# Kernel tuning notes

Measured on AMD Instinct MI355X. Metric: run time of the kernel, lower is better.

The kernel has to match this reference:

```python
import jax, jax.numpy as jnp
import numpy as np

C_IN = 96          # spectral bands
D2 = 2 * C_IN      # d = 192 (inner dim)
D4 = 4 * D2        # 768 (4-directional scan channels)
N = 16             # SSM state size
DR = 6             # delta_rank = ceil(96/16)
B, H, W = 2, 96, 96  # H,W not in {8,16,32,64} -> s=1 path


def setup_inputs() -> dict:
    key = jax.random.key(0)
    ks = jax.random.split(key, 8)
    g = lambda k, shape, s: jax.random.normal(k, shape, jnp.float32) * s
    return {
        "x": jax.random.normal(ks[0], (B, C_IN, H, W), jnp.float32),
        "W_in": g(ks[1], (C_IN, 2 * D2), 0.05),          # in_proj (in,out)
        "b_in": jnp.zeros((2 * D2,), jnp.float32),
        "w_dw": g(ks[2], (D2, 1, 3, 3), 0.1),            # depthwise conv OIHW
        "b_dw": jnp.zeros((D2,), jnp.float32),
        "A_log": jnp.log(jnp.tile(jnp.arange(1.0, N + 1.0, dtype=jnp.float32), (D4, 1))),
        "Dp": jnp.ones((D4,), jnp.float32),
        "W_x": g(ks[3], (D4, DR + 2 * N), 0.05),         # x_proj, no bias
        "W_delta": g(ks[4], (DR, D4), 0.1),
        "b_delta": g(ks[5], (D4,), 0.1),
        "ln_g": jnp.ones((D2,), jnp.float32),
        "ln_b": jnp.zeros((D2,), jnp.float32),
        "W_out": g(ks[6], (D2, C_IN), 0.05),             # out_proj, no bias
    }


def _selective_scan(u, delta, A, Bm, Cm, Dv):
    # u, delta: [b,L,d4]; Bm, Cm: [b,L,n]; A: [d4,n]; Dv: [d4]
    b, L, d4 = u.shape
    n = A.shape[1]

    def step(h, inps):
        u_t, dt, B_t, C_t = inps                      # [b,d4],[b,d4],[b,n],[b,n]
        dA = jnp.exp(dt[:, :, None] * A)              # [b,d4,n]
        h = dA * h + (dt * u_t)[:, :, None] * B_t[:, None, :]
        y = jnp.einsum('bdn,bn->bd', h, C_t) + Dv * u_t
        return h, y

    h0 = jnp.zeros((b, d4, n), u.dtype)
    xs = (jnp.swapaxes(u, 0, 1), jnp.swapaxes(delta, 0, 1),
          jnp.swapaxes(Bm, 0, 1), jnp.swapaxes(Cm, 0, 1))
    _, ys = jax.lax.scan(step, h0, xs)                # ys: [L,b,d4]
    return jnp.swapaxes(ys, 0, 1)                     # [b,L,d4]


def reference(x, W_in, b_in, w_dw, b_dw, A_log, Dp, W_x, W_delta, b_delta, ln_g, ln_b, W_out):
    b, c, Hh, Ww = x.shape                            # s = 1 (H not in {8,16,32,64})
    d = W_in.shape[1] // 2
    # in_proj on channel-last, chunk into x / gate z
    xz = jnp.einsum('bchw,ce->bhwe', x, W_in) + b_in  # [b,h,w,2d]
    xx, z = jnp.split(xz, 2, axis=-1)
    # depthwise conv + silu
    xc = jnp.transpose(xx, (0, 3, 1, 2))              # [b,d,h,w]
    xc = jax.lax.conv_general_dilated(
        xc, w_dw, (1, 1), 'SAME', feature_group_count=d,
        dimension_numbers=('NCHW', 'OIHW', 'NCHW')) + b_dw[None, :, None, None]
    xc = jax.nn.silu(xc)
    # 4 directional flattenings (with s=1: x1==x2 row-major, x3==x4 reversed)
    L = Hh * Ww
    flat = xc.reshape(b, d, L)
    flipped = xc[:, :, ::-1, ::-1].reshape(b, d, L)
    xl = jnp.swapaxes(jnp.concatenate([flat, flat, flipped, flipped], axis=1), 1, 2)  # [b,L,4d]
    # SSM parameterization
    A = -jnp.exp(A_log)                               # [4d,n]
    x_dbl = xl @ W_x                                  # [b,L,dr+2n]
    dr, n = W_delta.shape[0], A.shape[1]
    dt_r = x_dbl[..., :dr]
    Bm = x_dbl[..., dr:dr + n]
    Cm = x_dbl[..., dr + n:]
    delta = jax.nn.softplus(dt_r @ W_delta + b_delta)  # [b,L,4d]
    y = _selective_scan(xl, delta, A, Bm, Cm, Dp)      # [b,L,4d]
    # merge 4 directions back to spatial
    y = jnp.transpose(y.reshape(b, L, 4, d), (0, 2, 3, 1))  # [b,4,d,L]
    y1 = y[:, 0].reshape(b, d, Hh, Ww)
    y2 = y[:, 1].reshape(b, d, Hh, Ww)
    y3 = y[:, 2].reshape(b, d, Hh, Ww)[:, :, ::-1, ::-1]
    y4 = y[:, 3].reshape(b, d, Hh, Ww)[:, :, ::-1, ::-1]
    yh = jnp.transpose(y1 + y2 + y3 + y4, (0, 2, 3, 1))  # [b,h,w,d]
    # LayerNorm over d
    mu = yh.mean(-1, keepdims=True)
    var = ((yh - mu) ** 2).mean(-1, keepdims=True)
    yn = (yh - mu) * jax.lax.rsqrt(var + 1e-5) * ln_g + ln_b
    out = (yn * jax.nn.silu(z)) @ W_out               # [b,h,w,c]
    return jnp.transpose(out, (0, 3, 1, 2))           # [b,c,h,w]
```

## Files before the change

### kernel.cpp

```cpp
#include <hip/hip_runtime.h>
#include <hip/hip_bf16.h>
#include <math.h>

#define CIN 96
#define D2 192
#define D4 768
#define LL 9216
#define NN 16
#define NCH 288
#define CLEN 32

typedef float v2f __attribute__((ext_vector_type(2)));

#define SZ_Y4SLOT (2u*2u*9216u*192u)
#define SZ_BL    (2u*9216u*192u)
#define SZ_XDBL  (2u*9216u*38u)
#define SZ_S     (2u*4u*288u*192u)
#define SZ_HSLOT (2u*4u*288u*192u*8u)
#define F_Y4     0u
#define F_XX     0u
#define F_ZS     (F_Y4 + SZ_Y4SLOT)
#define F_XT     (F_ZS + SZ_BL)
#define F_XD0    (F_XT + SZ_BL)
#define F_XD1    (F_XD0 + SZ_XDBL)
#define F_XD2    (F_XD1 + SZ_XDBL)
#define F_XD3    (F_XD2 + SZ_XDBL)
#define F_SBUF   (F_XD3 + SZ_XDBL)
#define F_HBUF   (F_SBUF + SZ_S)
#define F_WCOMB  (F_HBUF + SZ_HSLOT)
#define F_A0     (F_WCOMB + 15360u)
#define F_FF     (F_A0 + 768u)

__device__ __forceinline__ float silu_f(float z) {
    return z / (1.0f + __expf(-z));
}

__global__ __launch_bounds__(256) void k0_foldw(
    const float* __restrict__ Wx, const float* __restrict__ Alog,
    float* __restrict__ wcomb, float* __restrict__ A0f, float* __restrict__ Ffl)
{
    int i = blockIdx.x * 256 + threadIdx.x;
    if (i < 768) {
        float a0 = -__expf(Alog[i * 16]);
        bool fast = true;
        for (int n = 1; n < 16; n++) {
            float an = -__expf(Alog[i * 16 + n]);
            float tgt = (n + 1) * a0;
            fast = fast && (fabsf(an - tgt) <= 1e-5f * fabsf(tgt));
        }
        A0f[i] = a0;
        Ffl[i] = fast ? 1.f : 0.f;
    }
    if (i >= 192 * 80) return;
    int d = i / 80, j = i % 80;
    float v = 0.f;
    if (j < 38) v = Wx[d * 38 + j] + Wx[(d + 192) * 38 + j];
    else if (j >= 40 && j < 78) {
        int jj = j - 40;
        v = Wx[(d + 384) * 38 + jj] + Wx[(d + 576) * 38 + jj];
    }
    wcomb[i] = v;
}

__global__ __launch_bounds__(256) void k1_inproj(
    const float* __restrict__ x, const float* __restrict__ Win,
    const float* __restrict__ bin, float* __restrict__ xx, float* __restrict__ zs)
{
    __shared__ float xs[32][68];
    __shared__ float wsh[32][100];
    int tid = threadIdx.x;
    int bid = blockIdx.x;
    int eq = bid & 3;
    int lt = (bid >> 2) % 144;
    int b = bid / 576;
    int l0 = lt * 64;
    int e0 = eq * 96;

    int lg = tid & 15;
    int cg = tid >> 4;
    v2f acc[4][3];
#pragma unroll
    for (int i = 0; i < 4; i++)
#pragma unroll
        for (int p = 0; p < 3; p++) { acc[i][p].x = 0.f; acc[i][p].y = 0.f; }

    for (int kc = 0; kc < 96; kc += 32) {
        __syncthreads();
        for (int i = tid; i < 512; i += 256) {
            int kk = i >> 4, q = i & 15;
            float4 v = *(const float4*)&x[(size_t)(b * 96 + kc + kk) * LL + l0 + q * 4];
            *(float4*)&xs[kk][q * 4] = v;
        }
        for (int i = tid; i < 768; i += 256) {
            int kk = i / 24, q = i - kk * 24;
            float4 v = *(const float4*)&Win[(kc + kk) * 384 + e0 + q * 4];
            *(float4*)&wsh[kk][q * 4] = v;
        }
        __syncthreads();
#pragma unroll 4
        for (int k = 0; k < 32; k++) {
            float4 xv = *(const float4*)&xs[k][lg * 4];
            const v2f* wp = (const v2f*)&wsh[k][cg * 6];
            v2f w0 = wp[0], w1 = wp[1], w2 = wp[2];
            float xa[4] = {xv.x, xv.y, xv.z, xv.w};
#pragma unroll
            for (int i = 0; i < 4; i++) {
                v2f xi; xi.x = xa[i]; xi.y = xa[i];
                acc[i][0] += xi * w0;
                acc[i][1] += xi * w1;
                acc[i][2] += xi * w2;
            }
        }
    }
    if (eq < 2) {
#pragma unroll
        for (int j = 0; j < 6; j++) {
            int e = e0 + cg * 6 + j;
            float bb = bin[e];
            float4 v = {acc[0][j >> 1][j & 1] + bb, acc[1][j >> 1][j & 1] + bb,
                        acc[2][j >> 1][j & 1] + bb, acc[3][j >> 1][j & 1] + bb};
            *(float4*)&xx[(size_t)(b * 192 + e) * LL + l0 + lg * 4] = v;
        }
    } else {
        int zc0 = e0 - 192 + cg * 6;
        float bb[6];
#pragma unroll
        for (int j = 0; j < 6; j++) bb[j] = bin[e0 + cg * 6 + j];
#pragma unroll
        for (int i = 0; i < 4; i++) {
            int l = l0 + lg * 4 + i;
            float* zp = &zs[((size_t)b * LL + l) * 192 + zc0];
#pragma unroll
            for (int p = 0; p < 3; p++) {
                float2 v;
                v.x = silu_f(acc[i][p].x + bb[2 * p]);
                v.y = silu_f(acc[i][p].y + bb[2 * p + 1]);
                *(float2*)&zp[2 * p] = v;
            }
        }
    }
}

__global__ __launch_bounds__(192) void k2_conv(
    const float* __restrict__ xx, const float* __restrict__ wdw,
    const float* __restrict__ bdw, float* __restrict__ xt)
{
    __shared__ float tile[32][97];
    __shared__ float wsm[32][9];
    __shared__ float bs[32];
    int tid = threadIdx.x;
    int bid = blockIdx.x;
    int h = bid % 96;
    int r = bid / 96;
    int dg = r % 6;
    int b = r / 6;

    for (int i = tid; i < 288; i += 192) wsm[i / 9][i % 9] = wdw[(dg * 32 + i / 9) * 9 + (i % 9)];
    if (tid < 32) bs[tid] = bdw[dg * 32 + tid];
    __syncthreads();

    int w = tid % 96;
    int dhalf = tid / 96;
    for (int p = 0; p < 16; p++) {
        int dsub = 2 * p + dhalf;
        const float* base = xx + (size_t)(b * 192 + dg * 32 + dsub) * LL;
        float acc = bs[dsub];
#pragma unroll
        for (int kh = 0; kh < 3; kh++) {
            int hh = h + kh - 1;
            if (hh < 0 || hh >= 96) continue;
            const float* row = base + hh * 96;
#pragma unroll
            for (int kw = 0; kw < 3; kw++) {
                int ww = w + kw - 1;
                if (ww < 0 || ww >= 96) continue;
                acc += row[ww] * wsm[dsub][kh * 3 + kw];
            }
        }
        tile[dsub][w] = silu_f(acc);
    }
    __syncthreads();
    for (int i = tid; i < 768; i += 192) {
        int q = i & 7, ls = i >> 3;
        float4 v = {tile[q * 4 + 0][ls], tile[q * 4 + 1][ls], tile[q * 4 + 2][ls], tile[q * 4 + 3][ls]};
        *(float4*)&xt[((size_t)b * LL + h * 96 + ls) * 192 + dg * 32 + q * 4] = v;
    }
}

__global__ __launch_bounds__(320) void k3_xdbl(
    const float* __restrict__ xt, const float* __restrict__ wcomb,
    float* __restrict__ xa0, float* __restrict__ xa1,
    float* __restrict__ xb0, float* __restrict__ xb1)
{
    __shared__ float xs[16][68];
    __shared__ float wsh[16][80];
    int tid = threadIdx.x;
    int bid = blockIdx.x;
    int kh = bid & 1;
    int rt = (bid >> 1) % 144;
    int b = bid / 288;
    int r0 = rt * 64;
    int k0 = kh * 96;
    float* __restrict__ xa = kh ? xa1 : xa0;
    float* __restrict__ xb = kh ? xb1 : xb0;

    int rg = tid / 20;
    int cg = tid % 20;
    v2f acc[4][2];
#pragma unroll
    for (int i = 0; i < 4; i++)
#pragma unroll
        for (int p = 0; p < 2; p++) { acc[i][p].x = 0.f; acc[i][p].y = 0.f; }

    for (int kc = 0; kc < 96; kc += 16) {
        __syncthreads();
        if (tid < 256) {
            int row = tid >> 2, dq = tid & 3;
            float4 v = *(const float4*)&xt[((size_t)b * LL + r0 + row) * 192 + k0 + kc + dq * 4];
            xs[dq * 4 + 0][row] = v.x;
            xs[dq * 4 + 1][row] = v.y;
            xs[dq * 4 + 2][row] = v.z;
            xs[dq * 4 + 3][row] = v.w;
        }
        for (int i = tid; i < 16 * 80; i += 320) {
            int d = i / 80, j = i - d * 80;
            wsh[d][j] = wcomb[(k0 + kc + d) * 80 + j];
        }
        __syncthreads();
#pragma unroll
        for (int d = 0; d < 16; d++) {
            float4 xv = *(const float4*)&xs[d][rg * 4];
            float4 wv = *(const float4*)&wsh[d][cg * 4];
            v2f w01; w01.x = wv.x; w01.y = wv.y;
            v2f w23; w23.x = wv.z; w23.y = wv.w;
            float xr[4] = {xv.x, xv.y, xv.z, xv.w};
#pragma unroll
            for (int i = 0; i < 4; i++) {
                v2f xi; xi.x = xr[i]; xi.y = xr[i];
                acc[i][0] += xi * w01;
                acc[i][1] += xi * w23;
            }
        }
    }
    int c0 = cg * 4;
#pragma unroll
    for (int i = 0; i < 4; i++) {
        int la = r0 + rg * 4 + i;
#pragma unroll
        for (int j = 0; j < 4; j++) {
            int col = c0 + j;
            float v = acc[i][j >> 1][j & 1];
            if (col < 38) {
                xa[((size_t)b * LL + la) * 38 + col] = v;
            } else if (col >= 40 && col < 78) {
                int lb = LL - 1 - la;
                xb[((size_t)b * LL + lb) * 38 + (col - 40)] = v;
            }
        }
    }
}

__global__ __launch_bounds__(192, 4) void k4_pass1(
    const float* __restrict__ xt,
    const float* __restrict__ xa0, const float* __restrict__ xa1,
    const float* __restrict__ xb0, const float* __restrict__ xb1,
    const float* __restrict__ Wd, const float* __restrict__ bdl,
    const float* __restrict__ Alog, const float* __restrict__ A0f,
    const float* __restrict__ Ffl,
    float* __restrict__ Sbuf, __hip_bfloat16* __restrict__ Hbuf)
{
    __shared__ float Bt[CLEN][16];
    __shared__ float Dt[CLEN][6];
    int tid = threadIdx.x;
    int bid = blockIdx.x;
    int k = bid % NCH;
    int r = bid / NCH;
    int dir = r & 3;
    int b = r >> 2;
    int l0 = k * CLEN;
    for (int i = tid; i < CLEN * 16; i += 192) {
        int t = i >> 4, n = i & 15;
        size_t rb = ((size_t)b * LL + l0 + t) * 38 + 6 + n;
        Bt[t][n] = (xa0[rb] + xa1[rb]) + (xb0[rb] + xb1[rb]);
    }
    for (int i = tid; i < CLEN * 6; i += 192) {
        int t = i / 6, rr = i - 6 * t;
        size_t rb = ((size_t)b * LL + l0 + t) * 38 + rr;
        Dt[t][rr] = (xa0[rb] + xa1[rb]) + (xb0[rb] + xb1[rb]);
    }
    __syncthreads();
    int c = tid;
    int d4 = dir * 192 + c;
    float a0 = A0f[d4];
    bool fast = (Ffl[d4] != 0.f);
    float wd[6];
#pragma unroll
    for (int rr = 0; rr < 6; rr++) wd[rr] = Wd[rr * 768 + d4];
    float bde = bdl[d4];
    float S = 0.f;
    int start = (dir < 2) ? l0 : (LL - 1 - l0);
    ptrdiff_t stp = (dir < 2) ? 192 : -192;
    const float* up = xt + (size_t)b * LL * 192 + (size_t)start * 192 + c;
    int bd = b * 4 + dir;
    size_t base = (((size_t)bd * NCH + k) * 192 + c) * 16;
    if (fast) {
        v2f h2[8];
#pragma unroll
        for (int n = 0; n < 8; n++) { h2[n].x = 0.f; h2[n].y = 0.f; }
#pragma unroll 2
        for (int t = 0; t < CLEN; t++) {
            float2 d01 = *(const float2*)&Dt[t][0];
            float2 d23 = *(const float2*)&Dt[t][2];
            float2 d45 = *(const float2*)&Dt[t][4];
            float s = bde + d01.x * wd[0] + d01.y * wd[1] + d23.x * wd[2]
                          + d23.y * wd[3] + d45.x * wd[4] + d45.y * wd[5];
            float dt = (s > 20.f) ? s : __logf(1.f + __expf(s));
            S += dt;
            float u = *up; up += stp;
            float du = dt * u;
            float e1 = __expf(dt * a0);
            float e2 = e1 * e1;
            v2f q; q.x = e1; q.y = e2;
            v2f e2v; e2v.x = e2; e2v.y = e2;
            v2f e4v = e2v * e2v;
            v2f q2 = q * e2v;
            v2f du2; du2.x = du; du2.y = du;
#pragma unroll
            for (int g = 0; g < 4; g++) {
                float4 bq = *(const float4*)&Bt[t][4 * g];
                v2f b0; b0.x = bq.x; b0.y = bq.y;
                v2f b1; b1.x = bq.z; b1.y = bq.w;
                h2[2 * g]     = q  * h2[2 * g]     + du2 * b0;
                h2[2 * g + 1] = q2 * h2[2 * g + 1] + du2 * b1;
                if (g < 3) { q *= e4v; q2 *= e4v; }
            }
        }
        __hip_bfloat16* hb = Hbuf + base;
#pragma unroll
        for (int n = 0; n < 8; n++) {
            hb[2 * n]     = __float2bfloat16(h2[n].x);
            hb[2 * n + 1] = __float2bfloat16(h2[n].y);
        }
    } else {
        float h[16];
#pragma unroll
        for (int n = 0; n < 16; n++) h[n] = 0.f;
        for (int t = 0; t < CLEN; t++) {
            float s = bde;
#pragma unroll
            for (int rr = 0; rr < 6; rr++) s += Dt[t][rr] * wd[rr];
            float dt = (s > 20.f) ? s : __logf(1.f + __expf(s));
            S += dt;
            float u = *up; up += stp;
            float du = dt * u;
#pragma unroll
            for (int n = 0; n < 16; n++) {
                float e = __expf(dt * (-__expf(Alog[d4 * 16 + n])));
                h[n] = e * h[n] + du * Bt[t][n];
            }
        }
#pragma unroll
        for (int n = 0; n < 16; n++) Hbuf[base + n] = __float2bfloat16(h[n]);
    }
    Sbuf[((size_t)bd * NCH + k) * 192 + c] = S;
}

__global__ __launch_bounds__(256) void k4_pass2(
    const float* __restrict__ Sbuf, const float* __restrict__ Alog,
    __hip_bfloat16* __restrict__ Hbuf)
{
    int lane = blockIdx.x * 256 + threadIdx.x;
    int bd = lane / 3072;
    int cn = lane % 3072;
    int c = cn >> 4, n = cn & 15;
    int dir = bd & 3;
    float an = -__expf(Alog[(dir * 192 + c) * 16 + n]);
    float h = 0.f;
#pragma unroll 8
    for (int k = 0; k < NCH; k++) {
        size_t sidx = ((size_t)bd * NCH + k) * 192 + c;
        float S = Sbuf[sidx];
        size_t idx = sidx * 16 + n;
        float hl = __bfloat162float(Hbuf[idx]);
        float P = __expf(an * S);
        Hbuf[idx] = __float2bfloat16(h);
        h = P * h + hl;
    }
}

__global__ __launch_bounds__(192, 4) void k4_pass3(
    const float* __restrict__ xt,
    const float* __restrict__ xa0, const float* __restrict__ xa1,
    const float* __restrict__ xb0, const float* __restrict__ xb1,
    const float* __restrict__ Wd, const float* __restrict__ bdl,
    const float* __restrict__ Alog, const float* __restrict__ A0f,
    const float* __restrict__ Ffl, const float* __restrict__ Dp,
    const __hip_bfloat16* __restrict__ Hbuf, __hip_bfloat16* __restrict__ y4)
{
    __shared__ float Bt[CLEN][16];
    __shared__ float Ct[CLEN][16];
    __shared__ float Dt[CLEN][6];
    int tid = threadIdx.x;
    int bid = blockIdx.x;
    int k = bid % NCH;
    int r = bid / NCH;
    int dir = r & 3;
    int b = r >> 2;
    int l0 = k * CLEN;
    for (int i = tid; i < CLEN * 16; i += 192) {
        int t = i >> 4, n = i & 15;
        size_t rb = ((size_t)b * LL + l0 + t) * 38;
        size_t r1 = rb + 6 + n, r2 = rb + 22 + n;
        Bt[t][n] = (xa0[r1] + xa1[r1]) + (xb0[r1] + xb1[r1]);
        Ct[t][n] = (xa0[r2] + xa1[r2]) + (xb0[r2] + xb1[r2]);
    }
    for (int i = tid; i < CLEN * 6; i += 192) {
        int t = i / 6, rr = i - 6 * t;
        size_t rb = ((size_t)b * LL + l0 + t) * 38 + rr;
        Dt[t][rr] = (xa0[rb] + xa1[rb]) + (xb0[rb] + xb1[rb]);
    }
    __syncthreads();
    int c = tid;
    int d4 = dir * 192 + c;
    float a0 = A0f[d4];
    bool fast = (Ffl[d4] != 0.f);
    float wd[6];
#pragma unroll
    for (int rr = 0; rr < 6; rr++) wd[rr] = Wd[rr * 768 + d4];
    float bde = bdl[d4];
    float Dv = Dp[d4];
    int bd = b * 4 + dir;
    size_t base = (((size_t)bd * NCH + k) * 192 + c) * 16;
    int start = (dir < 2) ? l0 : (LL - 1 - l0);
    ptrdiff_t stp = (dir < 2) ? 192 : -192;
    const float* up = xt + (size_t)b * LL * 192 + (size_t)start * 192 + c;
    __hip_bfloat16* yp = y4 + (size_t)bd * LL * 192 + (size_t)start * 192 + c;
    ptrdiff_t ystp = stp;
    if (fast) {
        v2f h2[8];
        const __hip_bfloat16* hb = Hbuf + base;
#pragma unroll
        for (int n = 0; n < 8; n++) {
            h2[n].x = __bfloat162float(hb[2 * n]);
            h2[n].y = __bfloat162float(hb[2 * n + 1]);
        }
#pragma unroll 2
        for (int t = 0; t < CLEN; t++) {
            float2 d01 = *(const float2*)&Dt[t][0];
            float2 d23 = *(const float2*)&Dt[t][2];
            float2 d45 = *(const float2*)&Dt[t][4];
            float s = bde + d01.x * wd[0] + d01.y * wd[1] + d23.x * wd[2]
                          + d23.y * wd[3] + d45.x * wd[4] + d45.y * wd[5];
            float dt = (s > 20.f) ? s : __logf(1.f + __expf(s));
            float u = *up; up += stp;
            float du = dt * u;
            float e1 = __expf(dt * a0);
            float e2 = e1 * e1;
            v2f q; q.x = e1; q.y = e2;
            v2f e2v; e2v.x = e2; e2v.y = e2;
            v2f e4v = e2v * e2v;
            v2f q2 = q * e2v;
            v2f du2; du2.x = du; du2.y = du;
            v2f ya; ya.x = 0.f; ya.y = 0.f;
            v2f yb; yb.x = 0.f; yb.y = 0.f;
#pragma unroll
            for (int g = 0; g < 4; g++) {
                float4 bq = *(const float4*)&Bt[t][4 * g];
                float4 cq = *(const float4*)&Ct[t][4 * g];
                v2f b0; b0.x = bq.x; b0.y = bq.y;
                v2f b1; b1.x = bq.z; b1.y = bq.w;
                v2f c0v; c0v.x = cq.x; c0v.y = cq.y;
                v2f c1v; c1v.x = cq.z; c1v.y = cq.w;
                h2[2 * g]     = q  * h2[2 * g]     + du2 * b0;
                ya += h2[2 * g] * c0v;
                h2[2 * g + 1] = q2 * h2[2 * g + 1] + du2 * b1;
                yb += h2[2 * g + 1] * c1v;
                if (g < 3) { q *= e4v; q2 *= e4v; }
            }
            float yv = (ya.x + ya.y) + (yb.x + yb.y) + Dv * u;
            *yp = __float2bfloat16(yv); yp += ystp;
        }
    } else {
        float h[16];
#pragma unroll
        for (int n = 0; n < 16; n++) h[n] = __bfloat162float(Hbuf[base + n]);
        for (int t = 0; t < CLEN; t++) {
            float s = bde;
#pragma unroll
            for (int rr = 0; rr < 6; rr++) s += Dt[t][rr] * wd[rr];
            float dt = (s > 20.f) ? s : __logf(1.f + __expf(s));
            float u = *up; up += stp;
            float du = dt * u;
            float yv = Dv * u;
#pragma unroll
            for (int n = 0; n < 16; n++) {
                float e = __expf(dt * (-__expf(Alog[d4 * 16 + n])));
                h[n] = e * h[n] + du * Bt[t][n];
                yv += h[n] * Ct[t][n];
            }
            *yp = __float2bfloat16(yv); yp += ystp;
        }
    }
}

__global__ __launch_bounds__(256) void k5_out(
    const __hip_bfloat16* __restrict__ y4, const float* __restrict__ zs,
    const float* __restrict__ lng, const float* __restrict__ lnb,
    const float* __restrict__ Wout, float* __restrict__ out)
{
    __shared__ float acts[16][196];
    __shared__ float wsh[32][100];
    int tid = threadIdx.x;
    int wv = tid >> 6;
    int lane = tid & 63;
    int gl0 = blockIdx.x * 16;
    int b = gl0 / LL;
    int l0 = gl0 % LL;
    const size_t ds = (size_t)LL * 192;

    for (int i = 0; i < 4; i++) {
        int rrow = wv * 4 + i;
        int l = l0 + rrow;
        float yv[3], zv[3];
        float s1 = 0.f, s2 = 0.f;
#pragma unroll
        for (int kk = 0; kk < 3; kk++) {
            int c = lane + kk * 64;
            size_t off = ((size_t)(b * 4) * LL + l) * 192 + c;
            float y = __bfloat162float(y4[off]) + __bfloat162float(y4[off + ds])
                    + __bfloat162float(y4[off + 2 * ds]) + __bfloat162float(y4[off + 3 * ds]);
            yv[kk] = y;
            zv[kk] = zs[((size_t)b * LL + l) * 192 + c];
            s1 += y; s2 += y * y;
        }
#pragma unroll
        for (int o = 32; o; o >>= 1) {
            s1 += __shfl_xor(s1, o, 64);
            s2 += __shfl_xor(s2, o, 64);
        }
        float mean = s1 * (1.f / 192.f);
        float var = s2 * (1.f / 192.f) - mean * mean;
        float rs = rsqrtf(var + 1e-5f);
#pragma unroll
        for (int kk = 0; kk < 3; kk++) {
            int c = lane + kk * 64;
            float yn = (yv[kk] - mean) * rs * lng[c] + lnb[c];
            acts[rrow][c] = yn * zv[kk];
        }
    }

    int ty = tid & 15;
    int tx = tid >> 4;
    v2f o2[3];
    o2[0].x = 0.f; o2[0].y = 0.f;
    o2[1].x = 0.f; o2[1].y = 0.f;
    o2[2].x = 0.f; o2[2].y = 0.f;

    for (int kc = 0; kc < 192; kc += 32) {
        __syncthreads();
        for (int i = tid; i < 32 * 24; i += 256) {
            int d = i / 24, q = i - d * 24;
            *(float4*)&wsh[d][q * 4] = *(const float4*)&Wout[(kc + d) * 96 + q * 4];
        }
        __syncthreads();
#pragma unroll
        for (int kk = 0; kk < 32; kk++) {
            float av = acts[ty][kc + kk];
            const v2f* wp = (const v2f*)&wsh[kk][tx * 6];
            v2f w0 = wp[0], w1 = wp[1], w2 = wp[2];
            v2f sp; sp.x = av; sp.y = av;
            o2[0] += sp * w0;
            o2[1] += sp * w1;
            o2[2] += sp * w2;
        }
    }
    int l = l0 + ty;
#pragma unroll
    for (int j = 0; j < 6; j++) {
        int n = tx * 6 + j;
        out[((size_t)(b * 96) + n) * LL + l] = o2[j >> 1][j & 1];
    }
}

extern "C" void kernel_launch(void* const* d_in, const int* in_sizes, int n_in,
                              void* d_out, int out_size, void* d_ws, size_t ws_size,
                              hipStream_t stream)
{
    const float* x    = (const float*)d_in[0];
    const float* Win  = (const float*)d_in[1];
    const float* bin  = (const float*)d_in[2];
    const float* wdw  = (const float*)d_in[3];
    const float* bdw  = (const float*)d_in[4];
    const float* Alog = (const float*)d_in[5];
    const float* Dp   = (const float*)d_in[6];
    const float* Wx   = (const float*)d_in[7];
    const float* Wd   = (const float*)d_in[8];
    const float* bdl  = (const float*)d_in[9];
    const float* lng  = (const float*)d_in[10];
    const float* lnb  = (const float*)d_in[11];
    const float* Wout = (const float*)d_in[12];
    float* out = (float*)d_out;

    float* ws    = (float*)d_ws;
    __hip_bfloat16* y4 = (__hip_bfloat16*)(ws + F_Y4);
    float* xx    = ws + F_XX;
    float* zs    = ws + F_ZS;
    float* xt    = ws + F_XT;
    float* xd0   = ws + F_XD0;
    float* xd1   = ws + F_XD1;
    float* xd2   = ws + F_XD2;
    float* xd3   = ws + F_XD3;
    float* Sbuf  = ws + F_SBUF;
    __hip_bfloat16* Hbuf = (__hip_bfloat16*)(ws + F_HBUF);
    float* wcomb = ws + F_WCOMB;
    float* A0f   = ws + F_A0;
    float* Ffl   = ws + F_FF;

    k0_foldw<<<60, 256, 0, stream>>>(Wx, Alog, wcomb, A0f, Ffl);
    k1_inproj<<<1152, 256, 0, stream>>>(x, Win, bin, xx, zs);
    k2_conv<<<1152, 192, 0, stream>>>(xx, wdw, bdw, xt);
    k3_xdbl<<<576, 320, 0, stream>>>(xt, wcomb, xd0, xd1, xd2, xd3);
    k4_pass1<<<2304, 192, 0, stream>>>(xt, xd0, xd1, xd2, xd3, Wd, bdl, Alog, A0f, Ffl, Sbuf, Hbuf);
    k4_pass2<<<96, 256, 0, stream>>>(Sbuf, Alog, Hbuf);
    k4_pass3<<<2304, 192, 0, stream>>>(xt, xd0, xd1, xd2, xd3, Wd, bdl, Alog, A0f, Ffl, Dp, Hbuf, y4);
    k5_out<<<1152, 256, 0, stream>>>(y4, zs, lng, lnb, Wout, out);
}
```

Before: 287.5 us.

## Emit local scan outputs in pass1 and add carry-in correction in pass3

Measured after the change: 290.2 us. About the same (+0.9%).

```diff
diff --git a/kernel.cpp b/kernel.cpp
--- a/kernel.cpp
+++ b/kernel.cpp
@@ -64,7 +64,8 @@
 
 __global__ __launch_bounds__(256) void k1_inproj(
     const float* __restrict__ x, const float* __restrict__ Win,
-    const float* __restrict__ bin, float* __restrict__ xx, float* __restrict__ zs)
+    const float* __restrict__ bin, float* __restrict__ xx,
+    __hip_bfloat16* __restrict__ zs)
 {
     __shared__ float xs[32][68];
     __shared__ float wsh[32][100];
@@ -129,13 +130,13 @@
 #pragma unroll
         for (int i = 0; i < 4; i++) {
             int l = l0 + lg * 4 + i;
-            float* zp = &zs[((size_t)b * LL + l) * 192 + zc0];
+            __hip_bfloat16* zp = &zs[((size_t)b * LL + l) * 192 + zc0];
 #pragma unroll
             for (int p = 0; p < 3; p++) {
-                float2 v;
-                v.x = silu_f(acc[i][p].x + bb[2 * p]);
-                v.y = silu_f(acc[i][p].y + bb[2 * p + 1]);
-                *(float2*)&zp[2 * p] = v;
+                __hip_bfloat162 hv = __halves2bfloat162(
+                    __float2bfloat16(silu_f(acc[i][p].x + bb[2 * p])),
+                    __float2bfloat16(silu_f(acc[i][p].y + bb[2 * p + 1])));
+                *(__hip_bfloat162*)&zp[2 * p] = hv;
             }
         }
     }
@@ -260,16 +261,18 @@
     }
 }
 
-__global__ __launch_bounds__(192, 4) void k4_pass1(
+__global__ __launch_bounds__(192, 4) void k4_scan(
     const float* __restrict__ xt,
     const float* __restrict__ xa0, const float* __restrict__ xa1,
     const float* __restrict__ xb0, const float* __restrict__ xb1,
     const float* __restrict__ Wd, const float* __restrict__ bdl,
     const float* __restrict__ Alog, const float* __restrict__ A0f,
-    const float* __restrict__ Ffl,
-    float* __restrict__ Sbuf, __hip_bfloat16* __restrict__ Hbuf)
+    const float* __restrict__ Ffl, const float* __restrict__ Dp,
+    float* __restrict__ Sbuf, __hip_bfloat16* __restrict__ Hbuf,
+    __hip_bfloat16* __restrict__ y4)
 {
     __shared__ float Bt[CLEN][16];
+    __shared__ float Ct[CLEN][16];
     __shared__ float Dt[CLEN][6];
     int tid = threadIdx.x;
     int bid = blockIdx.x;
@@ -280,8 +283,10 @@
     int l0 = k * CLEN;
     for (int i = tid; i < CLEN * 16; i += 192) {
         int t = i >> 4, n = i & 15;
-        size_t rb = ((size_t)b * LL + l0 + t) * 38 + 6 + n;
-        Bt[t][n] = (xa0[rb] + xa1[rb]) + (xb0[rb] + xb1[rb]);
+        size_t rb = ((size_t)b * LL + l0 + t) * 38;
+        size_t r1 = rb + 6 + n, r2 = rb + 22 + n;
+        Bt[t][n] = (xa0[r1] + xa1[r1]) + (xb0[r1] + xb1[r1]);
+        Ct[t][n] = (xa0[r2] + xa1[r2]) + (xb0[r2] + xb1[r2]);
     }
     for (int i = tid; i < CLEN * 6; i += 192) {
         int t = i / 6, rr = i - 6 * t;
@@ -297,12 +302,14 @@
 #pragma unroll
     for (int rr = 0; rr < 6; rr++) wd[rr] = Wd[rr * 768 + d4];
     float bde = bdl[d4];
+    float Dv = Dp[d4];
     float S = 0.f;
+    int bd = b * 4 + dir;
+    size_t base = (((size_t)bd * NCH + k) * 192 + c) * 16;
     int start = (dir < 2) ? l0 : (LL - 1 - l0);
     ptrdiff_t stp = (dir < 2) ? 192 : -192;
     const float* up = xt + (size_t)b * LL * 192 + (size_t)start * 192 + c;
-    int bd = b * 4 + dir;
-    size_t base = (((size_t)bd * NCH + k) * 192 + c) * 16;
+    __hip_bfloat16* yp = y4 + (size_t)bd * LL * 192 + (size_t)start * 192 + c;
     if (fast) {
         v2f h2[8];
 #pragma unroll
@@ -325,15 +332,24 @@
             v2f e4v = e2v * e2v;
             v2f q2 = q * e2v;
             v2f du2; du2.x = du; du2.y = du;
+            v2f ya; ya.x = 0.f; ya.y = 0.f;
+            v2f yb; yb.x = 0.f; yb.y = 0.f;
 #pragma unroll
             for (int g = 0; g < 4; g++) {
                 float4 bq = *(const float4*)&Bt[t][4 * g];
+                float4 cq = *(const float4*)&Ct[t][4 * g];
                 v2f b0; b0.x = bq.x; b0.y = bq.y;
                 v2f b1; b1.x = bq.z; b1.y = bq.w;
+                v2f c0v; c0v.x = cq.x; c0v.y = cq.y;
+                v2f c1v; c1v.x = cq.z; c1v.y = cq.w;
                 h2[2 * g]     = q  * h2[2 * g]     + du2 * b0;
+                ya += h2[2 * g] * c0v;
                 h2[2 * g + 1] = q2 * h2[2 * g + 1] + du2 * b1;
+                yb += h2[2 * g + 1] * c1v;
                 if (g < 3) { q *= e4v; q2 *= e4v; }
             }
+            float yv = (ya.x + ya.y) + (yb.x + yb.y) + Dv * u;
+            *yp = __float2bfloat16(yv); yp += stp;
         }
         __hip_bfloat16* hb = Hbuf + base;
 #pragma unroll
@@ -353,11 +369,14 @@
             S += dt;
             float u = *up; up += stp;
             float du = dt * u;
+            float yv = Dv * u;
 #pragma unroll
             for (int n = 0; n < 16; n++) {
                 float e = __expf(dt * (-__expf(Alog[d4 * 16 + n])));
                 h[n] = e * h[n] + du * Bt[t][n];
-            }
+                yv += h[n] * Ct[t][n];
+            }
+            *yp = __float2bfloat16(yv); yp += stp;
         }
 #pragma unroll
         for (int n = 0; n < 16; n++) Hbuf[base + n] = __float2bfloat16(h[n]);
@@ -388,16 +407,14 @@
     }
 }
 
-__global__ __launch_bounds__(192, 4) void k4_pass3(
-    const float* __restrict__ xt,
+__global__ __launch_bounds__(192, 4) void k4_corr(
     const float* __restrict__ xa0, const float* __restrict__ xa1,
     const float* __restrict__ xb0, const float* __restrict__ xb1,
     const float* __restrict__ Wd, const float* __restrict__ bdl,
     const float* __restrict__ Alog, const float* __restrict__ A0f,
-    const float* __restrict__ Ffl, const float* __restrict__ Dp,
+    const float* __restrict__ Ffl,
     const __hip_bfloat16* __restrict__ Hbuf, __hip_bfloat16* __restrict__ y4)
 {
-    __shared__ float Bt[CLEN][16];
     __shared__ float Ct[CLEN][16];
     __shared__ float Dt[CLEN][6];
     int tid = threadIdx.x;
@@ -406,13 +423,12 @@
     int r = bid / NCH;
     int dir = r & 3;
     int b = r >> 2;
+    if (k == 0) return;
     int l0 = k * CLEN;
     for (int i = tid; i < CLEN * 16; i += 192) {
         int t = i >> 4, n = i & 15;
-        size_t rb = ((size_t)b * LL + l0 + t) * 38;
-        size_t r1 = rb + 6 + n, r2 = rb + 22 + n;
-        Bt[t][n] = (xa0[r1] + xa1[r1]) + (xb0[r1] + xb1[r1]);
-        Ct[t][n] = (xa0[r2] + xa1[r2]) + (xb0[r2] + xb1[r2]);
+        size_t rb = ((size_t)b * LL + l0 + t) * 38 + 22 + n;
+        Ct[t][n] = (xa0[rb] + xa1[rb]) + (xb0[rb] + xb1[rb]);
     }
     for (int i = tid; i < CLEN * 6; i += 192) {
         int t = i / 6, rr = i - 6 * t;
@@ -428,21 +444,19 @@
 #pragma unroll
     for (int rr = 0; rr < 6; rr++) wd[rr] = Wd[rr * 768 + d4];
     float bde = bdl[d4];
-    float Dv = Dp[d4];
     int bd = b * 4 + dir;
     size_t base = (((size_t)bd * NCH + k) * 192 + c) * 16;
     int start = (dir < 2) ? l0 : (LL - 1 - l0);
     ptrdiff_t stp = (dir < 2) ? 192 : -192;
-    const float* up = xt + (size_t)b * LL * 192 + (size_t)start * 192 + c;
     __hip_bfloat16* yp = y4 + (size_t)bd * LL * 192 + (size_t)start * 192 + c;
-    ptrdiff_t ystp = stp;
+    float cumS = 0.f;
     if (fast) {
-        v2f h2[8];
+        v2f g2[8];
         const __hip_bfloat16* hb = Hbuf + base;
 #pragma unroll
         for (int n = 0; n < 8; n++) {
-            h2[n].x = __bfloat162float(hb[2 * n]);
-            h2[n].y = __bfloat162float(hb[2 * n + 1]);
+            g2[n].x = __bfloat162float(hb[2 * n]);
+            g2[n].y = __bfloat162float(hb[2 * n + 1]);
         }
 #pragma unroll 2
         for (int t = 0; t < CLEN; t++) {
@@ -452,59 +466,52 @@
             float s = bde + d01.x * wd[0] + d01.y * wd[1] + d23.x * wd[2]
                           + d23.y * wd[3] + d45.x * wd[4] + d45.y * wd[5];
             float dt = (s > 20.f) ? s : __logf(1.f + __expf(s));
-            float u = *up; up += stp;
-            float du = dt * u;
-            float e1 = __expf(dt * a0);
+            cumS += dt;
+            float e1 = __expf(cumS * a0);
             float e2 = e1 * e1;
             v2f q; q.x = e1; q.y = e2;
             v2f e2v; e2v.x = e2; e2v.y = e2;
             v2f e4v = e2v * e2v;
             v2f q2 = q * e2v;
-            v2f du2; du2.x = du; du2.y = du;
-            v2f ya; ya.x = 0.f; ya.y = 0.f;
-            v2f yb; yb.x = 0.f; yb.y = 0.f;
+            v2f ca; ca.x = 0.f; ca.y = 0.f;
+            v2f cb; cb.x = 0.f; cb.y = 0.f;
 #pragma unroll
             for (int g = 0; g < 4; g++) {
-                float4 bq = *(const float4*)&Bt[t][4 * g];
                 float4 cq = *(const float4*)&Ct[t][4 * g];
-                v2f b0; b0.x = bq.x; b0.y = bq.y;
-                v2f b1; b1.x = bq.z; b1.y = bq.w;
                 v2f c0v; c0v.x = cq.x; c0v.y = cq.y;
                 v2f c1v; c1v.x = cq.z; c1v.y = cq.w;
-                h2[2 * g]     = q  * h2[2 * g]     + du2 * b0;
-                ya += h2[2 * g] * c0v;
-                h2[2 * g + 1] = q2 * h2[2 * g + 1] + du2 * b1;
-                yb += h2[2 * g + 1] * c1v;
+                ca += (q * g2[2 * g]) * c0v;
+                cb += (q2 * g2[2 * g + 1]) * c1v;
                 if (g < 3) { q *= e4v; q2 *= e4v; }
             }
-            float yv = (ya.x + ya.y) + (yb.x + yb.y) + Dv * u;
-            *yp = __float2bfloat16(yv); yp += ystp;
+            float corr = (ca.x + ca.y) + (cb.x + cb.y);
+            float yv = __bfloat162float(*yp) + corr;
+            *yp = __float2bfloat16(yv); yp += stp;
         }
     } else {
-        float h[16];
-#pragma unroll
-        for (int n = 0; n < 16; n++) h[n] = __bfloat162float(Hbuf[base + n]);
+        float g[16];
+#pragma unroll
+        for (int n = 0; n < 16; n++) g[n] = __bfloat162float(Hbuf[base + n]);
         for (int t = 0; t < CLEN; t++) {
             float s = bde;
 #pragma unroll
             for (int rr = 0; rr < 6; rr++) s += Dt[t][rr] * wd[rr];
             float dt = (s > 20.f) ? s : __logf(1.f + __expf(s));
-            float u = *up; up += stp;
-            float du = dt * u;
-            float yv = Dv * u;
+            cumS += dt;
+            float corr = 0.f;
 #pragma unroll
             for (int n = 0; n < 16; n++) {
-                float e = __expf(dt * (-__expf(Alog[d4 * 16 + n])));
-                h[n] = e * h[n] + du * Bt[t][n];
-                yv += h[n] * Ct[t][n];
-            }
-            *yp = __float2bfloat16(yv); yp += ystp;
+                float an = -__expf(Alog[d4 * 16 + n]);
+                corr += g[n] * __expf(cumS * an) * Ct[t][n];
+            }
+            float yv = __bfloat162float(*yp) + corr;
+            *yp = __float2bfloat16(yv); yp += stp;
         }
     }
 }
 
 __global__ __launch_bounds__(256) void k5_out(
-    const __hip_bfloat16* __restrict__ y4, const float* __restrict__ zs,
+    const __hip_bfloat16* __restrict__ y4, const __hip_bfloat16* __restrict__ zs,
     const float* __restrict__ lng, const float* __restrict__ lnb,
     const float* __restrict__ Wout, float* __restrict__ out)
 {
@@ -530,7 +537,7 @@
             float y = __bfloat162float(y4[off]) + __bfloat162float(y4[off + ds])
                     + __bfloat162float(y4[off + 2 * ds]) + __bfloat162float(y4[off + 3 * ds]);
             yv[kk] = y;
-            zv[kk] = zs[((size_t)b * LL + l) * 192 + c];
+            zv[kk] = __bfloat162float(zs[((size_t)b * LL + l) * 192 + c]);
             s1 += y; s2 += y * y;
         }
 #pragma unroll
@@ -604,7 +611,7 @@
     float* ws    = (float*)d_ws;
     __hip_bfloat16* y4 = (__hip_bfloat16*)(ws + F_Y4);
     float* xx    = ws + F_XX;
-    float* zs    = ws + F_ZS;
+    __hip_bfloat16* zs = (__hip_bfloat16*)(ws + F_ZS);
     float* xt    = ws + F_XT;
     float* xd0   = ws + F_XD0;
     float* xd1   = ws + F_XD1;
@@ -620,8 +627,8 @@
     k1_inproj<<<1152, 256, 0, stream>>>(x, Win, bin, xx, zs);
     k2_conv<<<1152, 192, 0, stream>>>(xx, wdw, bdw, xt);
     k3_xdbl<<<576, 320, 0, stream>>>(xt, wcomb, xd0, xd1, xd2, xd3);
-    k4_pass1<<<2304, 192, 0, stream>>>(xt, xd0, xd1, xd2, xd3, Wd, bdl, Alog, A0f, Ffl, Sbuf, Hbuf);
+    k4_scan<<<2304, 192, 0, stream>>>(xt, xd0, xd1, xd2, xd3, Wd, bdl, Alog, A0f, Ffl, Dp, Sbuf, Hbuf, y4);
     k4_pass2<<<96, 256, 0, stream>>>(Sbuf, Alog, Hbuf);
-    k4_pass3<<<2304, 192, 0, stream>>>(xt, xd0, xd1, xd2, xd3, Wd, bdl, Alog, A0f, Ffl, Dp, Hbuf, y4);
+    k4_corr<<<2304, 192, 0, stream>>>(xd0, xd1, xd2, xd3, Wd, bdl, Alog, A0f, Ffl, Hbuf, y4);
     k5_out<<<1152, 256, 0, stream>>>(y4, zs, lng, lnb, Wout, out);
 }
```
